# Kernel optimization log

Measured on AMD Instinct MI355X. Metric: run time of the kernel, lower is better.

The kernel has to match this reference:

```python
import jax, jax.numpy as jnp
import numpy as np

N = 50000
E = 800000
IN_C, HID, OUT_C, HEADS = 128, 16, 64, 4
NEG_SLOPE = 0.2


def _gat_conv(x, src, dst, W, a_src, a_dst, b, heads, concat):
    # x: [N, Fin]; W: [Fin, heads*Fout]; a_src/a_dst: [heads, Fout]; b: [out]
    n = x.shape[0]
    h = (x @ W).reshape(n, heads, -1)                      # [N, H, F]
    alpha_s = jnp.einsum('nhf,hf->nh', h, a_src)           # [N, H]
    alpha_d = jnp.einsum('nhf,hf->nh', h, a_dst)
    e = jax.nn.leaky_relu(alpha_s[src] + alpha_d[dst], NEG_SLOPE)  # [E, H]
    m = jax.ops.segment_max(e, dst, num_segments=n)        # per-dest max (self-loops ensure nonempty)
    w = jnp.exp(e - m[dst])
    denom = jax.ops.segment_sum(w, dst, num_segments=n)
    alpha = w / (denom[dst] + 1e-16)                       # [E, H] segment softmax
    out = jax.ops.segment_sum(h[src] * alpha[:, :, None], dst, num_segments=n)  # [N, H, F]
    out = out.reshape(n, -1) if concat else out.mean(axis=1)
    return out + b


def setup_inputs() -> dict:
    key = jax.random.key(0)
    ks = jax.random.split(key, 16)
    x = jax.random.normal(ks[0], (N, IN_C), dtype=jnp.float32)
    edge_index = jax.random.randint(ks[1], (2, E), 0, N, dtype=jnp.int64)
    s = 0.1
    d = {'x': x, 'edge_index': edge_index}
    # layer 0: in=128 -> heads=4, F=16
    d['W0'] = jax.random.normal(ks[2], (IN_C, HEADS * HID), dtype=jnp.float32) * s
    d['as0'] = jax.random.normal(ks[3], (HEADS, HID), dtype=jnp.float32) * s
    d['ad0'] = jax.random.normal(ks[4], (HEADS, HID), dtype=jnp.float32) * s
    d['b0'] = jnp.zeros((HEADS * HID,), dtype=jnp.float32)
    # layer 1: in=64 -> heads=4, F=16
    d['W1'] = jax.random.normal(ks[5], (HEADS * HID, HEADS * HID), dtype=jnp.float32) * s
    d['as1'] = jax.random.normal(ks[6], (HEADS, HID), dtype=jnp.float32) * s
    d['ad1'] = jax.random.normal(ks[7], (HEADS, HID), dtype=jnp.float32) * s
    d['b1'] = jnp.zeros((HEADS * HID,), dtype=jnp.float32)
    # layer 2: in=64 -> heads=1, F=64, concat=False
    d['W2'] = jax.random.normal(ks[8], (HEADS * HID, OUT_C), dtype=jnp.float32) * s
    d['as2'] = jax.random.normal(ks[9], (1, OUT_C), dtype=jnp.float32) * s
    d['ad2'] = jax.random.normal(ks[10], (1, OUT_C), dtype=jnp.float32) * s
    d['b2'] = jnp.zeros((OUT_C,), dtype=jnp.float32)
    return d


def reference(x, edge_index, W0, as0, ad0, b0, W1, as1, ad1, b1, W2, as2, ad2, b2):
    loops = jnp.arange(N, dtype=edge_index.dtype)
    src = jnp.concatenate([edge_index[0], loops])  # PyG add_self_loops=True
    dst = jnp.concatenate([edge_index[1], loops])
    h = _gat_conv(x, src, dst, W0, as0, ad0, b0, HEADS, True)
    h = jax.nn.elu(h)
    h = _gat_conv(h, src, dst, W1, as1, ad1, b1, HEADS, True)
    h = jax.nn.elu(h)
    return _gat_conv(h, src, dst, W2, as2, ad2, b2, 1, False)
```

## Files before the change

### kernel.cpp

```cpp
#include <hip/hip_runtime.h>
#include <hip/hip_fp16.h>
#include <math.h>


#define NEG_SLOPE 0.2f
#define L1_CHUNK 4096


__global__ __launch_bounds__(256) void k_l1hist(
    const int* __restrict__ idx, int* __restrict__ ghist, int E, int etot) {
    __shared__ int h[256];
    const int t = threadIdx.x;
    h[t] = 0;
    __syncthreads();
    const int base = blockIdx.x * L1_CHUNK;
    for (int i = t; i < L1_CHUNK; i += 256) {
        int e = base + i;
        if (e >= etot) break;
        int dst = (e < E) ? idx[E + e] : (e - E);
        atomicAdd(&h[dst >> 8], 1);
    }
    __syncthreads();
    if (h[t]) atomicAdd(&ghist[t], h[t]);
}

__global__ __launch_bounds__(256) void k_scan256(
    const int* __restrict__ ghist, int* __restrict__ goff, int* __restrict__ gcur) {
    __shared__ int sc[256];
    const int t = threadIdx.x;
    int v = ghist[t];
    sc[t] = v;
    __syncthreads();
    for (int o = 1; o < 256; o <<= 1) {
        int x = (t >= o) ? sc[t - o] : 0;
        __syncthreads();
        sc[t] += x;
        __syncthreads();
    }
    int excl = sc[t] - v;
    goff[t] = excl;
    gcur[t] = excl;
    if (t == 255) goff[256] = sc[255];
}

__global__ __launch_bounds__(256) void k_l1scatter(
    const int* __restrict__ idx, int* __restrict__ gcur,
    unsigned long long* __restrict__ buf, int E, int etot) {
    __shared__ int h[256];
    __shared__ int lbase[256];
    const int t = threadIdx.x;
    h[t] = 0;
    __syncthreads();
    const int base = blockIdx.x * L1_CHUNK;
    for (int i = t; i < L1_CHUNK; i += 256) {
        int e = base + i;
        if (e >= etot) break;
        int dst = (e < E) ? idx[E + e] : (e - E);
        atomicAdd(&h[dst >> 8], 1);
    }
    __syncthreads();
    lbase[t] = h[t] ? atomicAdd(&gcur[t], h[t]) : 0;
    __syncthreads();
    h[t] = lbase[t];
    __syncthreads();
    for (int i = t; i < L1_CHUNK; i += 256) {
        int e = base + i;
        if (e >= etot) break;
        int dst, src;
        if (e < E) { dst = idx[E + e]; src = idx[e]; }
        else       { dst = src = e - E; }
        int pos = atomicAdd(&h[dst >> 8], 1);
        buf[pos] = ((unsigned long long)(unsigned)dst << 32) | (unsigned)src;
    }
}

__global__ __launch_bounds__(256) void k_l2build(
    const unsigned long long* __restrict__ buf, const int* __restrict__ goff,
    int* __restrict__ off, int* __restrict__ csr, int n, int etot) {
    __shared__ int sc[256];
    __shared__ int lcur[256];
    const int b = blockIdx.x, t = threadIdx.x;
    const int lo = goff[b], hi = goff[b + 1];
    sc[t] = 0;
    __syncthreads();
    for (int p = lo + t; p < hi; p += 256) {
        int dst = (int)(buf[p] >> 32);
        atomicAdd(&sc[dst & 255], 1);
    }
    __syncthreads();
    int v = sc[t];
    __syncthreads();
    sc[t] = v;
    __syncthreads();
    for (int o = 1; o < 256; o <<= 1) {
        int x = (t >= o) ? sc[t - o] : 0;
        __syncthreads();
        sc[t] += x;
        __syncthreads();
    }
    int excl = sc[t] - v;
    const int d = b * 256 + t;
    if (d < n) off[d] = lo + excl;
    lcur[t] = lo + excl;
    __syncthreads();
    for (int p = lo + t; p < hi; p += 256) {
        unsigned long long e = buf[p];
        int dst = (int)(e >> 32);
        int src = (int)(e & 0xffffffffu);
        int pos = atomicAdd(&lcur[dst & 255], 1);
        csr[pos] = src;
    }
    if (b == 0 && t == 0) off[n] = etot;
    if (b == 0 && t < 8) csr[etot + t] = 0;
}


template <int H>
__device__ __forceinline__ float4 aggq(
    const __half* __restrict__ h, const float* __restrict__ asb,
    const float* __restrict__ adb, const int* __restrict__ off,
    const int* __restrict__ csr, int node, int c4, int n) {
    const int head = (H == 1) ? 0 : (c4 >> 2);
    float den = 0.f;
    float4 acc = make_float4(0.f, 0.f, 0.f, 0.f);
    int p = 0, e = 0;
    float adn = 0.f;
    if (node < n) {
        p = off[node];
        e = off[node + 1];
        adn = adb[node * H + head];
    }
    int s0 = csr[p], s1 = csr[p + 1], s2 = csr[p + 2], s3 = csr[p + 3];
    float a0 = asb[s0 * H + head];
    float a1 = asb[s1 * H + head];
    uint2 v0 = *(const uint2*)(h + (size_t)s0 * 64 + c4 * 4);
    uint2 v1 = *(const uint2*)(h + (size_t)s1 * 64 + c4 * 4);
    while (__any(p < e)) {
        const bool q0 = p < e;
        const bool q1 = (p + 1) < e;
        const int s4 = csr[p + 4];
        const int s5 = csr[p + 5];
        const float a2 = asb[s2 * H + head];
        const float a3 = asb[s3 * H + head];
        const uint2 v2 = *(const uint2*)(h + (size_t)s2 * 64 + c4 * 4);
        const uint2 v3 = *(const uint2*)(h + (size_t)s3 * 64 + c4 * 4);
        {
            float ev = a0 + adn;
            ev = ev > 0.f ? ev : NEG_SLOPE * ev;
            const float wv = q0 ? __expf(ev) : 0.f;
            const float2 f01 = __half22float2(*(const __half2*)&v0.x);
            const float2 f23 = __half22float2(*(const __half2*)&v0.y);
            den += wv;
            acc.x = fmaf(wv, f01.x, acc.x);
            acc.y = fmaf(wv, f01.y, acc.y);
            acc.z = fmaf(wv, f23.x, acc.z);
            acc.w = fmaf(wv, f23.y, acc.w);
        }
        {
            float ev = a1 + adn;
            ev = ev > 0.f ? ev : NEG_SLOPE * ev;
            const float wv = q1 ? __expf(ev) : 0.f;
            const float2 f01 = __half22float2(*(const __half2*)&v1.x);
            const float2 f23 = __half22float2(*(const __half2*)&v1.y);
            den += wv;
            acc.x = fmaf(wv, f01.x, acc.x);
            acc.y = fmaf(wv, f01.y, acc.y);
            acc.z = fmaf(wv, f23.x, acc.z);
            acc.w = fmaf(wv, f23.y, acc.w);
        }
        p = q0 ? p + 2 : p;
        s0 = s2; s1 = s3; s2 = s4; s3 = s5;
        a0 = a2; a1 = a3;
        v0 = v2; v1 = v3;
    }
    const float inv = 1.f / (den + 1e-16f);
    return make_float4(acc.x * inv, acc.y * inv, acc.z * inv, acc.w * inv);
}

template <int K, int H, int F>
__global__ __launch_bounds__(256) void k_gemm_alpha(
    const float* __restrict__ x, const float* __restrict__ W,
    const float* __restrict__ a_s, const float* __restrict__ a_d,
    __half* __restrict__ h, float* __restrict__ as_o, float* __restrict__ ad_o,
    int n) {
    __shared__ float xs[16][K];
    const int tid = threadIdx.x;
    const int base = blockIdx.x * 16;
    int rows = n - base; if (rows > 16) rows = 16;
    const int kv = K / 4;
    for (int i = tid; i < rows * kv; i += 256) {
        int r = i / kv, c = i - r * kv;
        ((float4*)&xs[r][0])[c] = ((const float4*)(x + (size_t)(base + r) * K))[c];
    }
    __syncthreads();
    const int w = tid >> 6, lane = tid & 63;
    const int node0 = base + w * 4;
    float acc0 = 0.f, acc1 = 0.f, acc2 = 0.f, acc3 = 0.f;
    #pragma unroll 4
    for (int k = 0; k < K; ++k) {
        float wv = W[k * 64 + lane];
        acc0 = fmaf(xs[w * 4 + 0][k], wv, acc0);
        acc1 = fmaf(xs[w * 4 + 1][k], wv, acc1);
        acc2 = fmaf(xs[w * 4 + 2][k], wv, acc2);
        acc3 = fmaf(xs[w * 4 + 3][k], wv, acc3);
    }
    const int head = (H == 1) ? 0 : (lane >> 4);
    const int f = (H == 1) ? lane : (lane & (F - 1));
    const float asv = a_s[head * F + f];
    const float adv = a_d[head * F + f];
    float accs[4] = {acc0, acc1, acc2, acc3};
    #pragma unroll
    for (int j = 0; j < 4; ++j) {
        int node = node0 + j;
        if (node >= n) break;
        h[(size_t)node * 64 + lane] = __float2half_rn(accs[j]);
        float vs = accs[j] * asv;
        float vd = accs[j] * adv;
        #pragma unroll
        for (int o = F >> 1; o > 0; o >>= 1) {
            vs += __shfl_xor(vs, o);
            vd += __shfl_xor(vd, o);
        }
        if (f == 0) {
            as_o[node * H + head] = vs;
            ad_o[node * H + head] = vd;
        }
    }
}

template <int HA, int HG, int FG>
__global__ __launch_bounds__(256) void k_agg_gemm(
    const __half* __restrict__ h_in, const float* __restrict__ asb_in,
    const float* __restrict__ adb_in, const int* __restrict__ off,
    const int* __restrict__ csr, const float* __restrict__ bias,
    const float* __restrict__ W, const float* __restrict__ a_s,
    const float* __restrict__ a_d, __half* __restrict__ h_out,
    float* __restrict__ asb_out, float* __restrict__ adb_out, int n) {
    __shared__ float xs[16][64];
    const int tid = threadIdx.x;
    const int w = tid >> 6, lane = tid & 63;
    const int q = lane >> 4, c4 = lane & 15;
    const int base = blockIdx.x * 16;
    const int nodeA = base + w * 4 + q;
    float4 r = aggq<HA>(h_in, asb_in, adb_in, off, csr, nodeA, c4, n);
    if (nodeA < n) {
        const float4 bv = *(const float4*)(bias + c4 * 4);
        r.x += bv.x; r.y += bv.y; r.z += bv.z; r.w += bv.w;
        r.x = r.x > 0.f ? r.x : expm1f(r.x);
        r.y = r.y > 0.f ? r.y : expm1f(r.y);
        r.z = r.z > 0.f ? r.z : expm1f(r.z);
        r.w = r.w > 0.f ? r.w : expm1f(r.w);
        *(float4*)&xs[w * 4 + q][c4 * 4] = r;
    }
    __syncthreads();
    float acc0 = 0.f, acc1 = 0.f, acc2 = 0.f, acc3 = 0.f;
    #pragma unroll 4
    for (int k = 0; k < 64; ++k) {
        float wv = W[k * 64 + lane];
        acc0 = fmaf(xs[w * 4 + 0][k], wv, acc0);
        acc1 = fmaf(xs[w * 4 + 1][k], wv, acc1);
        acc2 = fmaf(xs[w * 4 + 2][k], wv, acc2);
        acc3 = fmaf(xs[w * 4 + 3][k], wv, acc3);
    }
    const int head = (HG == 1) ? 0 : (lane >> 4);
    const int f = (HG == 1) ? lane : (lane & (FG - 1));
    const float asv = a_s[head * FG + f];
    const float adv = a_d[head * FG + f];
    float accs[4] = {acc0, acc1, acc2, acc3};
    const int node0 = base + w * 4;
    #pragma unroll
    for (int j = 0; j < 4; ++j) {
        int node = node0 + j;
        if (node >= n) break;
        h_out[(size_t)node * 64 + lane] = __float2half_rn(accs[j]);
        float vs = accs[j] * asv;
        float vd = accs[j] * adv;
        #pragma unroll
        for (int o = FG >> 1; o > 0; o >>= 1) {
            vs += __shfl_xor(vs, o);
            vd += __shfl_xor(vd, o);
        }
        if (f == 0) {
            asb_out[node * HG + head] = vs;
            adb_out[node * HG + head] = vd;
        }
    }
}

__global__ __launch_bounds__(256) void k_agg_final(
    const __half* __restrict__ h, const float* __restrict__ asb,
    const float* __restrict__ adb, const int* __restrict__ off,
    const int* __restrict__ csr, const float* __restrict__ bias,
    float* __restrict__ out, int n) {
    const int tid = threadIdx.x;
    const int w = tid >> 6, lane = tid & 63;
    const int q = lane >> 4, c4 = lane & 15;
    const int node = blockIdx.x * 16 + w * 4 + q;
    float4 r = aggq<1>(h, asb, adb, off, csr, node, c4, n);
    if (node < n) {
        const float4 bv = *(const float4*)(bias + c4 * 4);
        r.x += bv.x; r.y += bv.y; r.z += bv.z; r.w += bv.w;
        *(float4*)(out + (size_t)node * 64 + c4 * 4) = r;
    }
}


extern "C" void kernel_launch(void* const* d_in, const int* in_sizes, int n_in,
                              void* d_out, int out_size, void* d_ws, size_t ws_size,
                              hipStream_t stream) {
    const float* x   = (const float*)d_in[0];
    const int*   idx = (const int*)d_in[1];
    const float* W0  = (const float*)d_in[2];
    const float* as0 = (const float*)d_in[3];
    const float* ad0 = (const float*)d_in[4];
    const float* b0  = (const float*)d_in[5];
    const float* W1  = (const float*)d_in[6];
    const float* as1 = (const float*)d_in[7];
    const float* ad1 = (const float*)d_in[8];
    const float* b1  = (const float*)d_in[9];
    const float* W2  = (const float*)d_in[10];
    const float* as2 = (const float*)d_in[11];
    const float* ad2 = (const float*)d_in[12];
    const float* b2  = (const float*)d_in[13];
    float* out = (float*)d_out;

    const int n    = in_sizes[0] / 128;
    const int E    = in_sizes[1] / 2;
    const int etot = E + n;

    char* p = (char*)d_ws;
    auto alloc = [&](size_t bytes) {
        char* r = p;
        p += (bytes + 255) & ~(size_t)255;
        return r;
    };
    int*    off   = (int*)alloc((size_t)(n + 1) * 4);
    int*    csr   = (int*)alloc((size_t)(etot + 8) * 4);
    int*    ghist = (int*)alloc(256 * 4);
    int*    goff  = (int*)alloc(257 * 4);
    int*    gcur  = (int*)alloc(256 * 4);
    float*  asbA  = (float*)alloc((size_t)n * 4 * 4);
    float*  adbA  = (float*)alloc((size_t)n * 4 * 4);
    float*  asbB  = (float*)alloc((size_t)n * 4 * 4);
    float*  adbB  = (float*)alloc((size_t)n * 4 * 4);
    __half* hA    = (__half*)alloc((size_t)n * 64 * 2);
    __half* hB    = (__half*)alloc((size_t)n * 64 * 2);
    unsigned long long* buf = (unsigned long long*)alloc((size_t)etot * 8);

    const int nb_l1 = (etot + L1_CHUNK - 1) / L1_CHUNK;
    const int nb_l2 = (n + 255) / 256;
    const int nb_g  = (n + 15) / 16;

    hipMemsetAsync(ghist, 0, 256 * 4, stream);
    k_l1hist<<<nb_l1, 256, 0, stream>>>(idx, ghist, E, etot);
    k_scan256<<<1, 256, 0, stream>>>(ghist, goff, gcur);
    k_l1scatter<<<nb_l1, 256, 0, stream>>>(idx, gcur, buf, E, etot);
    k_l2build<<<nb_l2, 256, 0, stream>>>(buf, goff, off, csr, n, etot);

    k_gemm_alpha<128, 4, 16><<<nb_g, 256, 0, stream>>>(x, W0, as0, ad0, hA, asbA, adbA, n);
    k_agg_gemm<4, 4, 16><<<nb_g, 256, 0, stream>>>(hA, asbA, adbA, off, csr, b0,
                                                   W1, as1, ad1, hB, asbB, adbB, n);
    k_agg_gemm<4, 1, 64><<<nb_g, 256, 0, stream>>>(hB, asbB, adbB, off, csr, b1,
                                                   W2, as2, ad2, hA, asbA, adbA, n);
    k_agg_final<<<nb_g, 256, 0, stream>>>(hA, asbA, adbA, off, csr, b2, out, n);
}
```

Baseline: 258.5 us.

## Sort nodes by in-degree and process aggregation in degree-sorted order

Builds a degree histogram during CSR construction, scans it, and scatters node ids into a permutation sorted by in-degree. The aggregation kernels then process nodes in that order so that lanes in a wavefront have similar edge counts, reducing divergence and tail imbalance. In exchange it adds two small kernels, an extra indirection load per node, and output writes that are less coalesced across nodes.

```diff
diff --git a/kernel.cpp b/kernel.cpp
--- a/kernel.cpp
+++ b/kernel.cpp
@@ -76,7 +76,8 @@
 
 __global__ __launch_bounds__(256) void k_l2build(
     const unsigned long long* __restrict__ buf, const int* __restrict__ goff,
-    int* __restrict__ off, int* __restrict__ csr, int n, int etot) {
+    int* __restrict__ off, int* __restrict__ csr, int* __restrict__ dhist,
+    int n, int etot) {
     __shared__ int sc[256];
     __shared__ int lcur[256];
     const int b = blockIdx.x, t = threadIdx.x;
@@ -100,7 +101,10 @@
     }
     int excl = sc[t] - v;
     const int d = b * 256 + t;
-    if (d < n) off[d] = lo + excl;
+    if (d < n) {
+        off[d] = lo + excl;
+        atomicAdd(&dhist[v > 255 ? 255 : v], 1);
+    }
     lcur[t] = lo + excl;
     __syncthreads();
     for (int p = lo + t; p < hi; p += 256) {
@@ -112,6 +116,48 @@
     }
     if (b == 0 && t == 0) off[n] = etot;
     if (b == 0 && t < 8) csr[etot + t] = 0;
+}
+
+__global__ __launch_bounds__(256) void k_degscan(
+    const int* __restrict__ dhist, int* __restrict__ dcur) {
+    __shared__ int sc[256];
+    const int t = threadIdx.x;
+    int v = dhist[t];
+    sc[t] = v;
+    __syncthreads();
+    for (int o = 1; o < 256; o <<= 1) {
+        int x = (t >= o) ? sc[t - o] : 0;
+        __syncthreads();
+        sc[t] += x;
+        __syncthreads();
+    }
+    dcur[t] = sc[t] - v;
+}
+
+__global__ __launch_bounds__(256) void k_permscatter(
+    const int* __restrict__ off, int* __restrict__ dcur,
+    int* __restrict__ perm, int n) {
+    __shared__ int h[256];
+    __shared__ int cur[256];
+    const int t = threadIdx.x;
+    h[t] = 0;
+    __syncthreads();
+    const int d = blockIdx.x * 256 + t;
+    int bin = -1;
+    if (d < n) {
+        int deg = off[d + 1] - off[d];
+        bin = deg > 255 ? 255 : deg;
+        atomicAdd(&h[bin], 1);
+    }
+    __syncthreads();
+    cur[t] = h[t] ? atomicAdd(&dcur[t], h[t]) : 0;
+    __syncthreads();
+    h[t] = cur[t];
+    __syncthreads();
+    if (d < n) {
+        int pos = atomicAdd(&h[bin], 1);
+        perm[pos] = d;
+    }
 }
 
 
@@ -232,16 +278,18 @@
 __global__ __launch_bounds__(256) void k_agg_gemm(
     const __half* __restrict__ h_in, const float* __restrict__ asb_in,
     const float* __restrict__ adb_in, const int* __restrict__ off,
-    const int* __restrict__ csr, const float* __restrict__ bias,
-    const float* __restrict__ W, const float* __restrict__ a_s,
-    const float* __restrict__ a_d, __half* __restrict__ h_out,
-    float* __restrict__ asb_out, float* __restrict__ adb_out, int n) {
+    const int* __restrict__ csr, const int* __restrict__ perm,
+    const float* __restrict__ bias, const float* __restrict__ W,
+    const float* __restrict__ a_s, const float* __restrict__ a_d,
+    __half* __restrict__ h_out, float* __restrict__ asb_out,
+    float* __restrict__ adb_out, int n) {
     __shared__ float xs[16][64];
     const int tid = threadIdx.x;
     const int w = tid >> 6, lane = tid & 63;
     const int q = lane >> 4, c4 = lane & 15;
     const int base = blockIdx.x * 16;
-    const int nodeA = base + w * 4 + q;
+    const int gA = base + w * 4 + q;
+    const int nodeA = (gA < n) ? perm[gA] : n;
     float4 r = aggq<HA>(h_in, asb_in, adb_in, off, csr, nodeA, c4, n);
     if (nodeA < n) {
         const float4 bv = *(const float4*)(bias + c4 * 4);
@@ -267,11 +315,11 @@
     const float asv = a_s[head * FG + f];
     const float adv = a_d[head * FG + f];
     float accs[4] = {acc0, acc1, acc2, acc3};
-    const int node0 = base + w * 4;
     #pragma unroll
     for (int j = 0; j < 4; ++j) {
-        int node = node0 + j;
-        if (node >= n) break;
+        const int gj = base + w * 4 + j;
+        if (gj >= n) break;
+        const int node = perm[gj];
         h_out[(size_t)node * 64 + lane] = __float2half_rn(accs[j]);
         float vs = accs[j] * asv;
         float vd = accs[j] * adv;
@@ -290,12 +338,13 @@
 __global__ __launch_bounds__(256) void k_agg_final(
     const __half* __restrict__ h, const float* __restrict__ asb,
     const float* __restrict__ adb, const int* __restrict__ off,
-    const int* __restrict__ csr, const float* __restrict__ bias,
-    float* __restrict__ out, int n) {
+    const int* __restrict__ csr, const int* __restrict__ perm,
+    const float* __restrict__ bias, float* __restrict__ out, int n) {
     const int tid = threadIdx.x;
     const int w = tid >> 6, lane = tid & 63;
     const int q = lane >> 4, c4 = lane & 15;
-    const int node = blockIdx.x * 16 + w * 4 + q;
+    const int g = blockIdx.x * 16 + w * 4 + q;
+    const int node = (g < n) ? perm[g] : n;
     float4 r = aggq<1>(h, asb, adb, off, csr, node, c4, n);
     if (node < n) {
         const float4 bv = *(const float4*)(bias + c4 * 4);
@@ -337,8 +386,11 @@
     int*    off   = (int*)alloc((size_t)(n + 1) * 4);
     int*    csr   = (int*)alloc((size_t)(etot + 8) * 4);
     int*    ghist = (int*)alloc(256 * 4);
+    int*    dhist = (int*)alloc(256 * 4);
     int*    goff  = (int*)alloc(257 * 4);
     int*    gcur  = (int*)alloc(256 * 4);
+    int*    dcur  = (int*)alloc(256 * 4);
+    int*    perm  = (int*)alloc((size_t)n * 4);
     float*  asbA  = (float*)alloc((size_t)n * 4 * 4);
     float*  adbA  = (float*)alloc((size_t)n * 4 * 4);
     float*  asbB  = (float*)alloc((size_t)n * 4 * 4);
@@ -351,16 +403,18 @@
     const int nb_l2 = (n + 255) / 256;
     const int nb_g  = (n + 15) / 16;
 
-    hipMemsetAsync(ghist, 0, 256 * 4, stream);
+    hipMemsetAsync(ghist, 0, 2 * 256 * 4, stream);
     k_l1hist<<<nb_l1, 256, 0, stream>>>(idx, ghist, E, etot);
     k_scan256<<<1, 256, 0, stream>>>(ghist, goff, gcur);
     k_l1scatter<<<nb_l1, 256, 0, stream>>>(idx, gcur, buf, E, etot);
-    k_l2build<<<nb_l2, 256, 0, stream>>>(buf, goff, off, csr, n, etot);
+    k_l2build<<<nb_l2, 256, 0, stream>>>(buf, goff, off, csr, dhist, n, etot);
+    k_degscan<<<1, 256, 0, stream>>>(dhist, dcur);
+    k_permscatter<<<nb_l2, 256, 0, stream>>>(off, dcur, perm, n);
 
     k_gemm_alpha<128, 4, 16><<<nb_g, 256, 0, stream>>>(x, W0, as0, ad0, hA, asbA, adbA, n);
-    k_agg_gemm<4, 4, 16><<<nb_g, 256, 0, stream>>>(hA, asbA, adbA, off, csr, b0,
+    k_agg_gemm<4, 4, 16><<<nb_g, 256, 0, stream>>>(hA, asbA, adbA, off, csr, perm, b0,
                                                    W1, as1, ad1, hB, asbB, adbB, n);
-    k_agg_gemm<4, 1, 64><<<nb_g, 256, 0, stream>>>(hB, asbB, adbB, off, csr, b1,
+    k_agg_gemm<4, 1, 64><<<nb_g, 256, 0, stream>>>(hB, asbB, adbB, off, csr, perm, b1,
                                                    W2, as2, ad2, hA, asbA, adbA, n);
-    k_agg_final<<<nb_g, 256, 0, stream>>>(hA, asbA, adbA, off, csr, b2, out, n);
-}
+    k_agg_final<<<nb_g, 256, 0, stream>>>(hA, asbA, adbA, off, csr, perm, b2, out, n);
+}
```

Measured after the change: 402.3 us. 55.7% more time.
